# Performance work log

Hardware: AMD Instinct MI355X
Metric: run time of the kernel (lower is better)

## Reference

```python
import jax, jax.numpy as jnp
import numpy as np
import math

N, S, C, K, V = 32, 4096, 1, 512, 128
TARGET_SCALE = 0.06  # normalize_scale == embedding_scale when normalize=True


def setup_inputs() -> dict:
    key = jax.random.key(0)
    k1, k2 = jax.random.split(key)
    x0 = jax.random.normal(k1, (N, S, C, V), dtype=jnp.float32)
    emb = jax.random.normal(k2, (C, K, V), dtype=jnp.float32) * TARGET_SCALE
    # after_update(): renormalize each code vector to norm = embedding_scale*sqrt(V)
    tn = TARGET_SCALE * math.sqrt(V)
    emb = emb * (tn / jnp.linalg.norm(emb, axis=2, keepdims=True))
    return {"x0": x0, "embedding0": emb}


def _vq_forward(x0, embedding0):
    tn = TARGET_SCALE * math.sqrt(V)
    # normalize inputs and codebook to the same norm (normalize=True path)
    x = tn * x0 / jnp.linalg.norm(x0, axis=3, keepdims=True)              # (N,S,C,V)
    emb = tn * embedding0 / jnp.linalg.norm(embedding0, axis=2, keepdims=True)  # (C,K,V)

    xf = x.reshape(N * S, C, V)
    x2 = jnp.sum(xf * xf, axis=2)                     # (NS, C)
    e2 = jnp.sum(emb * emb, axis=2)                   # (C, K)
    dots = jnp.einsum('ncv,ckv->nck', xf, emb)        # (NS, C, K)
    d2 = x2[:, :, None] + e2[None, :, :] - 2.0 * dots
    index = jnp.argmin(d2, axis=2)                    # (NS, C) int

    # entropy of code usage: histc over n_classes, normalized by len(index)=NS
    hist = jnp.zeros((K,), jnp.float32).at[index.reshape(-1)].add(1.0)
    prob = hist / float(N * S)
    entropy = -jnp.sum(jnp.where(hist > 0, prob * jnp.log(jnp.where(hist > 0, prob, 1.0)), 0.0))

    # gather selected code vectors per channel
    output = emb[jnp.arange(C)[None, :], index]       # (NS, C, V)
    output = output.reshape(x.shape)                  # (N,S,C,V)

    sg = jax.lax.stop_gradient
    out0 = sg(output - x) + x                                              # straight-through
    out1 = jnp.sum((sg(x) - output) ** 2, axis=3)                          # codebook loss (N,S,C)
    out2 = jnp.sum((x - sg(output)) ** 2, axis=3) + jnp.sum((x - x0) ** 2, axis=3)  # commitment + norm penalty
    return out0, out1, out2, entropy


def reference(x0, embedding0):
    return _vq_forward(x0, embedding0)
```

## Files before the change

kernel.cpp:

```cpp
#include <hip/hip_runtime.h>
#include <math.h>

#define VDIM   128
#define KCODES 512
#define NROWS  (32 * 4096)
#define TILE_ROWS 512
#define NBLK (NROWS / TILE_ROWS)
#define TN 0.67882250993908565f

typedef __attribute__((ext_vector_type(8))) short bf16x8;
typedef __attribute__((ext_vector_type(4))) float f32x4;

__device__ __forceinline__ unsigned short f2bf(float f) {
    unsigned u = __float_as_uint(f);
    unsigned r = u + 0x7FFFu + ((u >> 16) & 1u);
    return (unsigned short)(r >> 16);
}

__device__ __forceinline__ bf16x8 pack8(f32x4 a, f32x4 b) {
    bf16x8 v;
    v[0] = (short)f2bf(a[0]); v[1] = (short)f2bf(a[1]);
    v[2] = (short)f2bf(a[2]); v[3] = (short)f2bf(a[3]);
    v[4] = (short)f2bf(b[0]); v[5] = (short)f2bf(b[1]);
    v[6] = (short)f2bf(b[2]); v[7] = (short)f2bf(b[3]);
    return v;
}

__global__ void prep_emb(const float* __restrict__ emb0,
                         float* __restrict__ embn,
                         unsigned short* __restrict__ ebf) {
    int k = blockIdx.x;
    int l = threadIdx.x;
    const float* row = emb0 + (size_t)k * VDIM;
    float a = row[l];
    float b = row[l + 64];
    float ss = a * a + b * b;
    #pragma unroll
    for (int off = 32; off; off >>= 1) ss += __shfl_xor(ss, off);
    float nrm = sqrtf(ss);
    float ea = (TN * a) / nrm;
    float eb = (TN * b) / nrm;
    embn[(size_t)k * VDIM + l]      = ea;
    embn[(size_t)k * VDIM + l + 64] = eb;
    size_t base = ((size_t)(k >> 4) << 11) + ((size_t)(k & 15) << 3);
    int d1 = l;
    int d2 = l + 64;
    ebf[base + ((size_t)(d1 >> 3) << 7) + (d1 & 7)] = f2bf(ea);
    ebf[base + ((size_t)(d2 >> 3) << 7) + (d2 & 7)] = f2bf(eb);
}

__global__ __launch_bounds__(1024, 4) void vq_main(
        const float* __restrict__ x0,
        const unsigned short* __restrict__ ebf,
        const float* __restrict__ embn,
        unsigned* __restrict__ hist,
        float* __restrict__ out0,
        float* __restrict__ out1,
        float* __restrict__ out2) {
    __shared__ uint4 sB[8192];
    __shared__ int   sbesti[TILE_ROWS];
    __shared__ float sdot[TILE_ROWS];
    __shared__ float sn0[TILE_ROWS];

    int t = threadIdx.x;
    int w = t >> 6;
    int l = t & 63;
    int n15 = l & 15;
    int q = l >> 4;

    const uint4* ebg = (const uint4*)ebf;
    #pragma unroll
    for (int r = 0; r < 8; ++r)
        sB[(r << 10) + t] = ebg[(r << 10) + t];

    int rowbase = blockIdx.x * TILE_ROWS + (w << 5);
    bf16x8 afr[2][4];
    float nsq[2];
    #pragma unroll
    for (int s = 0; s < 2; ++s) {
        const float* xrow = x0 + (size_t)(rowbase + (s << 4) + n15) * VDIM + (q << 3);
        float p0 = 0.f, p1 = 0.f;
        #pragma unroll
        for (int kc = 0; kc < 4; ++kc) {
            const f32x4* xp = (const f32x4*)(xrow + (kc << 5));
            f32x4 a = __builtin_nontemporal_load(xp);
            f32x4 b = __builtin_nontemporal_load(xp + 1);
            p0 = fmaf(a[0], a[0], p0); p1 = fmaf(a[1], a[1], p1);
            p0 = fmaf(a[2], a[2], p0); p1 = fmaf(a[3], a[3], p1);
            p0 = fmaf(b[0], b[0], p0); p1 = fmaf(b[1], b[1], p1);
            p0 = fmaf(b[2], b[2], p0); p1 = fmaf(b[3], b[3], p1);
            afr[s][kc] = pack8(a, b);
        }
        nsq[s] = p0 + p1;
        nsq[s] += __shfl_xor(nsq[s], 16, 64);
        nsq[s] += __shfl_xor(nsq[s], 32, 64);
    }

    float best[2][4];
    int   bidx[2][4];
    #pragma unroll
    for (int s = 0; s < 2; ++s)
        #pragma unroll
        for (int r = 0; r < 4; ++r) { best[s][r] = -3.4e38f; bidx[s][r] = 0; }

    const f32x4 zero4 = {0.f, 0.f, 0.f, 0.f};

    __syncthreads();

    #pragma unroll 2
    for (int cn = 0; cn < 32; ++cn) {
        const bf16x8* bls = ((const bf16x8*)sB) + (cn << 8) + l;
        bf16x8 b0 = bls[0], b1 = bls[64], b2 = bls[128], b3 = bls[192];
        int nbase = (cn << 4) + n15;
        #pragma unroll
        for (int s = 0; s < 2; ++s) {
            f32x4 acc = __builtin_amdgcn_mfma_f32_16x16x32_bf16(afr[s][0], b0, zero4, 0, 0, 0);
            acc = __builtin_amdgcn_mfma_f32_16x16x32_bf16(afr[s][1], b1, acc, 0, 0, 0);
            acc = __builtin_amdgcn_mfma_f32_16x16x32_bf16(afr[s][2], b2, acc, 0, 0, 0);
            acc = __builtin_amdgcn_mfma_f32_16x16x32_bf16(afr[s][3], b3, acc, 0, 0, 0);
            #pragma unroll
            for (int r = 0; r < 4; ++r) {
                float d = acc[r];
                if (d > best[s][r]) { best[s][r] = d; bidx[s][r] = nbase; }
            }
        }
    }

    #pragma unroll
    for (int m = 1; m <= 8; m <<= 1) {
        #pragma unroll
        for (int s = 0; s < 2; ++s)
            #pragma unroll
            for (int r = 0; r < 4; ++r) {
                float ov = __shfl_xor(best[s][r], m, 64);
                int   oi = __shfl_xor(bidx[s][r], m, 64);
                if (ov > best[s][r] || (ov == best[s][r] && oi < bidx[s][r])) {
                    best[s][r] = ov; bidx[s][r] = oi;
                }
            }
    }

    if (n15 == 0) {
        #pragma unroll
        for (int s = 0; s < 2; ++s)
            #pragma unroll
            for (int r = 0; r < 4; ++r) {
                int lr = (w << 5) + (s << 4) + (q << 2) + r;
                sbesti[lr] = bidx[s][r];
                sdot[lr]   = best[s][r];
            }
    }
    if (q == 0) {
        #pragma unroll
        for (int s = 0; s < 2; ++s) sn0[(w << 5) + (s << 4) + n15] = nsq[s];
    }
    __syncthreads();

    size_t blockrow = (size_t)blockIdx.x * TILE_ROWS;
    #pragma unroll
    for (int pass = 0; pass < 16; ++pass) {
        int lr = (pass << 5) + (t >> 5);
        int v4 = t & 31;
        int bi = sbesti[lr];
        f32x4 e = *((const f32x4*)(embn + (size_t)bi * VDIM) + v4);
        __builtin_nontemporal_store(e, (f32x4*)(out0 + (blockrow + lr) * (size_t)VDIM) + v4);
    }

    if (t < TILE_ROWS) {
        size_t row = blockrow + t;
        int bi = sbesti[t];
        float dotv = sdot[t];
        float nn = sn0[t];
        float sc = TN / sqrtf(nn);
        float o1 = 2.f * TN * TN - 2.f * sc * dotv;
        __builtin_nontemporal_store(o1, &out1[row]);
        float sm = sc - 1.f;
        __builtin_nontemporal_store(o1 + sm * sm * nn, &out2[row]);
        atomicAdd(&hist[bi], 1u);
    }
}

__global__ void entropy_k(const unsigned* __restrict__ hist,
                          float* __restrict__ out) {
    __shared__ float red[8];
    int t = threadIdx.x;
    float h = (float)hist[t];
    float p = h / (float)NROWS;
    float term = (h > 0.f) ? p * logf(p) : 0.f;
    #pragma unroll
    for (int off = 32; off; off >>= 1) term += __shfl_xor(term, off);
    if ((t & 63) == 0) red[t >> 6] = term;
    __syncthreads();
    if (t == 0) {
        float ssum = 0.f;
        #pragma unroll
        for (int i = 0; i < 8; i++) ssum += red[i];
        out[0] = -ssum;
    }
}

extern "C" void kernel_launch(void* const* d_in, const int* in_sizes, int n_in,
                              void* d_out, int out_size, void* d_ws, size_t ws_size,
                              hipStream_t stream) {
    const float* x0   = (const float*)d_in[0];
    const float* emb0 = (const float*)d_in[1];

    float* embn = (float*)d_ws;
    unsigned* hist = (unsigned*)(embn + (size_t)KCODES * VDIM);
    unsigned short* ebf = (unsigned short*)(hist + KCODES);

    float* out  = (float*)d_out;
    float* out0 = out;
    float* out1 = out0 + (size_t)NROWS * VDIM;
    float* out2 = out1 + NROWS;
    float* oent = out2 + NROWS;

    hipMemsetAsync(hist, 0, KCODES * sizeof(unsigned), stream);
    prep_emb<<<KCODES, 64, 0, stream>>>(emb0, embn, ebf);
    vq_main<<<NBLK, 1024, 0, stream>>>(x0, ebf, embn, hist,
                                       out0, out1, out2);
    entropy_k<<<1, KCODES, 0, stream>>>(hist, oent);
}
```

Before: 175.1 us.

## Fuse codebook normalization into main kernel and use per-block histograms

Removes the separate prep_emb kernel and the memset by having every block normalize the codebook itself: it computes per-code scales into shared memory and builds the bf16 MFMA tile directly from the raw embedding. Histogram counts go to shared-memory atomics and are written as per-block partials, which the entropy kernel then reduces, so the global atomics go away. The x loads are issued early to overlap with the codebook preprocessing. In exchange, each of the 256 blocks repeats the full codebook normalization (256 KB read per block) and the out0 gather now scales values on the fly.

```diff
diff --git a/kernel.cpp b/kernel.cpp
--- a/kernel.cpp
+++ b/kernel.cpp
@@ -26,38 +26,16 @@
     return v;
 }
 
-__global__ void prep_emb(const float* __restrict__ emb0,
-                         float* __restrict__ embn,
-                         unsigned short* __restrict__ ebf) {
-    int k = blockIdx.x;
-    int l = threadIdx.x;
-    const float* row = emb0 + (size_t)k * VDIM;
-    float a = row[l];
-    float b = row[l + 64];
-    float ss = a * a + b * b;
-    #pragma unroll
-    for (int off = 32; off; off >>= 1) ss += __shfl_xor(ss, off);
-    float nrm = sqrtf(ss);
-    float ea = (TN * a) / nrm;
-    float eb = (TN * b) / nrm;
-    embn[(size_t)k * VDIM + l]      = ea;
-    embn[(size_t)k * VDIM + l + 64] = eb;
-    size_t base = ((size_t)(k >> 4) << 11) + ((size_t)(k & 15) << 3);
-    int d1 = l;
-    int d2 = l + 64;
-    ebf[base + ((size_t)(d1 >> 3) << 7) + (d1 & 7)] = f2bf(ea);
-    ebf[base + ((size_t)(d2 >> 3) << 7) + (d2 & 7)] = f2bf(eb);
-}
-
-__global__ __launch_bounds__(1024, 4) void vq_main(
+__global__ __launch_bounds__(1024, 4) void vq_fused(
         const float* __restrict__ x0,
-        const unsigned short* __restrict__ ebf,
-        const float* __restrict__ embn,
-        unsigned* __restrict__ hist,
+        const float* __restrict__ emb0,
+        unsigned short* __restrict__ hist_part,
         float* __restrict__ out0,
         float* __restrict__ out1,
         float* __restrict__ out2) {
     __shared__ uint4 sB[8192];
+    __shared__ float sscale[KCODES];
+    __shared__ int   shist[KCODES];
     __shared__ int   sbesti[TILE_ROWS];
     __shared__ float sdot[TILE_ROWS];
     __shared__ float sn0[TILE_ROWS];
@@ -68,23 +46,56 @@
     int n15 = l & 15;
     int q = l >> 4;
 
-    const uint4* ebg = (const uint4*)ebf;
-    #pragma unroll
-    for (int r = 0; r < 8; ++r)
-        sB[(r << 10) + t] = ebg[(r << 10) + t];
-
     int rowbase = blockIdx.x * TILE_ROWS + (w << 5);
+    f32x4 ax[2][4][2];
+    #pragma unroll
+    for (int s = 0; s < 2; ++s) {
+        const float* xrow = x0 + (size_t)(rowbase + (s << 4) + n15) * VDIM + (q << 3);
+        #pragma unroll
+        for (int kc = 0; kc < 4; ++kc) {
+            const f32x4* xp = (const f32x4*)(xrow + (kc << 5));
+            ax[s][kc][0] = __builtin_nontemporal_load(xp);
+            ax[s][kc][1] = __builtin_nontemporal_load(xp + 1);
+        }
+    }
+
+    if (t < KCODES) shist[t] = 0;
+
+    #pragma unroll 4
+    for (int i = 0; i < 32; ++i) {
+        int k = (w << 5) + i;
+        const float* row = emb0 + (size_t)k * VDIM;
+        float a = row[l];
+        float b = row[l + 64];
+        float ss = a * a + b * b;
+        #pragma unroll
+        for (int off = 32; off; off >>= 1) ss += __shfl_xor(ss, off);
+        if (l == 0) sscale[k] = TN / sqrtf(ss);
+    }
+    __syncthreads();
+
+    #pragma unroll
+    for (int i = 0; i < 8; ++i) {
+        int g = (i << 10) + t;
+        int k = ((g >> 8) << 4) | (g & 15);
+        int d0 = ((g >> 4) & 15) << 3;
+        float s = sscale[k];
+        const f32x4* ep = (const f32x4*)(emb0 + (size_t)k * VDIM + d0);
+        f32x4 a = ep[0], b = ep[1];
+        f32x4 as, bs;
+        as[0] = a[0] * s; as[1] = a[1] * s; as[2] = a[2] * s; as[3] = a[3] * s;
+        bs[0] = b[0] * s; bs[1] = b[1] * s; bs[2] = b[2] * s; bs[3] = b[3] * s;
+        ((bf16x8*)sB)[g] = pack8(as, bs);
+    }
+
     bf16x8 afr[2][4];
     float nsq[2];
     #pragma unroll
     for (int s = 0; s < 2; ++s) {
-        const float* xrow = x0 + (size_t)(rowbase + (s << 4) + n15) * VDIM + (q << 3);
         float p0 = 0.f, p1 = 0.f;
         #pragma unroll
         for (int kc = 0; kc < 4; ++kc) {
-            const f32x4* xp = (const f32x4*)(xrow + (kc << 5));
-            f32x4 a = __builtin_nontemporal_load(xp);
-            f32x4 b = __builtin_nontemporal_load(xp + 1);
+            f32x4 a = ax[s][kc][0], b = ax[s][kc][1];
             p0 = fmaf(a[0], a[0], p0); p1 = fmaf(a[1], a[1], p1);
             p0 = fmaf(a[2], a[2], p0); p1 = fmaf(a[3], a[3], p1);
             p0 = fmaf(b[0], b[0], p0); p1 = fmaf(b[1], b[1], p1);
@@ -162,8 +173,11 @@
         int lr = (pass << 5) + (t >> 5);
         int v4 = t & 31;
         int bi = sbesti[lr];
-        f32x4 e = *((const f32x4*)(embn + (size_t)bi * VDIM) + v4);
-        __builtin_nontemporal_store(e, (f32x4*)(out0 + (blockrow + lr) * (size_t)VDIM) + v4);
+        float s = sscale[bi];
+        f32x4 e = *((const f32x4*)(emb0 + (size_t)bi * VDIM) + v4);
+        f32x4 o;
+        o[0] = e[0] * s; o[1] = e[1] * s; o[2] = e[2] * s; o[3] = e[3] * s;
+        __builtin_nontemporal_store(o, (f32x4*)(out0 + (blockrow + lr) * (size_t)VDIM) + v4);
     }
 
     if (t < TILE_ROWS) {
@@ -176,20 +190,36 @@
         __builtin_nontemporal_store(o1, &out1[row]);
         float sm = sc - 1.f;
         __builtin_nontemporal_store(o1 + sm * sm * nn, &out2[row]);
-        atomicAdd(&hist[bi], 1u);
-    }
-}
-
-__global__ void entropy_k(const unsigned* __restrict__ hist,
-                          float* __restrict__ out) {
+        atomicAdd(&shist[bi], 1);
+    }
+    __syncthreads();
+
+    if (t < KCODES)
+        hist_part[((size_t)blockIdx.x << 9) + t] = (unsigned short)shist[t];
+}
+
+__global__ __launch_bounds__(1024) void entropy_k(
+        const unsigned short* __restrict__ hp,
+        float* __restrict__ out) {
+    __shared__ int   s2[1024];
     __shared__ float red[8];
     int t = threadIdx.x;
-    float h = (float)hist[t];
-    float p = h / (float)NROWS;
-    float term = (h > 0.f) ? p * logf(p) : 0.f;
-    #pragma unroll
-    for (int off = 32; off; off >>= 1) term += __shfl_xor(term, off);
-    if ((t & 63) == 0) red[t >> 6] = term;
+    int c = t & 511;
+    int half = t >> 9;
+    int sum = 0;
+    #pragma unroll 8
+    for (int b = half * 128; b < half * 128 + 128; ++b)
+        sum += hp[(b << 9) + c];
+    s2[t] = sum;
+    __syncthreads();
+    if (t < 512) {
+        float h = (float)(s2[t] + s2[t + 512]);
+        float p = h / (float)NROWS;
+        float term = (h > 0.f) ? p * logf(p) : 0.f;
+        #pragma unroll
+        for (int off = 32; off; off >>= 1) term += __shfl_xor(term, off);
+        if ((t & 63) == 0) red[t >> 6] = term;
+    }
     __syncthreads();
     if (t == 0) {
         float ssum = 0.f;
@@ -205,9 +235,7 @@
     const float* x0   = (const float*)d_in[0];
     const float* emb0 = (const float*)d_in[1];
 
-    float* embn = (float*)d_ws;
-    unsigned* hist = (unsigned*)(embn + (size_t)KCODES * VDIM);
-    unsigned short* ebf = (unsigned short*)(hist + KCODES);
+    unsigned short* hist_part = (unsigned short*)d_ws;
 
     float* out  = (float*)d_out;
     float* out0 = out;
@@ -215,9 +243,6 @@
     float* out2 = out1 + NROWS;
     float* oent = out2 + NROWS;
 
-    hipMemsetAsync(hist, 0, KCODES * sizeof(unsigned), stream);
-    prep_emb<<<KCODES, 64, 0, stream>>>(emb0, embn, ebf);
-    vq_main<<<NBLK, 1024, 0, stream>>>(x0, ebf, embn, hist,
-                                       out0, out1, out2);
-    entropy_k<<<1, KCODES, 0, stream>>>(hist, oent);
-}
+    vq_fused<<<NBLK, 1024, 0, stream>>>(x0, emb0, hist_part, out0, out1, out2);
+    entropy_k<<<1, 1024, 0, stream>>>(hist_part, oent);
+}
```

Result: faster. 166.5 us (-4.9%).
